# Performance work log

Measured on AMD Instinct MI355X. Metric: run time of the kernel, lower is better.

## Reference

```python
import jax, jax.numpy as jnp
import numpy as np

B = 32768
IN_DIM = 768
HIDDENS = [2048, 1024, 512]
EMBED_DIM = 128
NUM_EMB = 1024
DEPTH = 3


def setup_inputs() -> dict:
    key = jax.random.key(0)
    ks = jax.random.split(key, 20)
    d = {"x": jax.random.normal(ks[0], (B, IN_DIM), dtype=jnp.float32)}
    # Encoder: in -> h0 -> h1 -> h2 -> embed  (weights stored as [in, out])
    enc_dims = [IN_DIM] + HIDDENS + [EMBED_DIM]
    for i in range(4):
        fan_in = enc_dims[i]
        d[f"enc_W{i+1}"] = jax.random.normal(ks[1 + i], (enc_dims[i], enc_dims[i + 1]), dtype=jnp.float32) / np.sqrt(fan_in)
        d[f"enc_b{i+1}"] = jnp.zeros((enc_dims[i + 1],), dtype=jnp.float32)
    # Decoder: embed -> h0 -> h1 -> h2 -> in
    dec_dims = [EMBED_DIM] + HIDDENS + [IN_DIM]
    for i in range(4):
        fan_in = dec_dims[i]
        d[f"dec_W{i+1}"] = jax.random.normal(ks[5 + i], (dec_dims[i], dec_dims[i + 1]), dtype=jnp.float32) / np.sqrt(fan_in)
        d[f"dec_b{i+1}"] = jnp.zeros((dec_dims[i + 1],), dtype=jnp.float32)
    # Codebook (nn.Embedding weight, initialized ~ N(0,1) as in the module)
    d["codebook"] = jax.random.normal(ks[9], (NUM_EMB, EMBED_DIM), dtype=jnp.float32)
    return d


def _encoder(x, W1, b1, W2, b2, W3, b3, W4, b4):
    x = jax.nn.relu(x @ W1 + b1)
    x = jax.nn.relu(x @ W2 + b2)
    x = jax.nn.relu(x @ W3 + b3)
    return x @ W4 + b4


def _decoder(x, W1, b1, W2, b2, W3, b3, W4, b4):
    x = jax.nn.relu(x @ W1 + b1)
    x = jax.nn.relu(x @ W2 + b2)
    x = jax.nn.relu(x @ W3 + b3)
    return x @ W4 + b4


def reference(x,
              enc_W1, enc_b1, enc_W2, enc_b2, enc_W3, enc_b3, enc_W4, enc_b4,
              dec_W1, dec_b1, dec_W2, dec_b2, dec_W3, dec_b3, dec_W4, dec_b4,
              codebook):
    z = _encoder(x, enc_W1, enc_b1, enc_W2, enc_b2, enc_W3, enc_b3, enc_W4, enc_b4)
    z_det = jax.lax.stop_gradient(z)

    cb_sq = jnp.sum(codebook * codebook, axis=1)  # [K]
    residue = z_det
    z_hat = jnp.zeros_like(z_det)
    codes = []
    for _ in range(DEPTH):  # residual quantization loop
        # squared L2 distances [B, K]
        dist = (jnp.sum(residue * residue, axis=1, keepdims=True)
                + cb_sq
                - 2.0 * residue @ codebook.T)
        idx = jnp.argmin(dist, axis=1)          # [B]
        codes.append(idx)
        z_hat = z_hat + codebook[idx]           # gather codebook vectors
        residue = z_det - z_hat
    all_codes = jnp.stack(codes, axis=1)        # [B, DEPTH] int

    # straight-through estimator: forward uses z_hat, grad flows through z
    z_flow = z + jax.lax.stop_gradient(z_hat - z)
    x_recon = _decoder(z_flow, dec_W1, dec_b1, dec_W2, dec_b2, dec_W3, dec_b3, dec_W4, dec_b4)
    return (x_recon, all_codes)
```

## Files before the change

kernel.cpp:

```cpp
#include <hip/hip_runtime.h>

#define FLT_MAX_C 3.402823466e+38f

typedef __attribute__((ext_vector_type(8))) __bf16 bf16x8;
typedef __attribute__((ext_vector_type(4))) float f32x4;

static __device__ __forceinline__ ushort f2bf(float x) {
    union { float f; unsigned u; } v; v.f = x;
    unsigned r = (v.u + 0x7FFFu + ((v.u >> 16) & 1u)) >> 16;
    return (ushort)r;
}

static __device__ __forceinline__ void xcd_swz(int& bx, int& by) {
    const int gx = gridDim.x;
    const int nwg = gx * gridDim.y;
    const int bid = blockIdx.y * gx + blockIdx.x;
    const int q = nwg >> 3, r = nwg & 7;
    const int xcd = bid & 7, lid = bid >> 3;
    const int swz = (xcd < r ? xcd * (q + 1) : r * (q + 1) + (xcd - r) * q) + lid;
    bx = swz % gx;
    by = swz / gx;
}

template<bool RELU>
__device__ __forceinline__ void gemm_f32_dev(
    const float* __restrict__ A, const float* __restrict__ W,
    const float* __restrict__ bias, float* __restrict__ C, int K, int N,
    int bxi, int byi)
{
    __shared__ float As[8][128];
    __shared__ float Bs[8][132];
    const int tid = threadIdx.x;
    const int bm = byi << 7;
    const int bn = bxi << 7;

    const int la_row = tid >> 1;
    const int la_k   = (tid & 1) << 2;
    const int lb_row = tid >> 5;
    const int lb_col = (tid & 31) << 2;
    const int tm4 = (tid >> 4) << 2;
    const int tn4 = (tid & 15) << 2;

    float acc[8][8];
    #pragma unroll
    for (int i = 0; i < 8; ++i)
        #pragma unroll
        for (int j = 0; j < 8; ++j) acc[i][j] = 0.f;

    const float* aptr = A + (size_t)(bm + la_row) * K + la_k;
    const float* bptr = W + (size_t)lb_row * N + bn + lb_col;

    float4 av = *(const float4*)(aptr);
    float4 bv = *(const float4*)(bptr);

    for (int k0 = 0; k0 < K; k0 += 8) {
        __syncthreads();
        As[la_k + 0][la_row] = av.x;
        As[la_k + 1][la_row] = av.y;
        As[la_k + 2][la_row] = av.z;
        As[la_k + 3][la_row] = av.w;
        *(float4*)(&Bs[lb_row][lb_col]) = bv;
        __syncthreads();
        if (k0 + 8 < K) {
            av = *(const float4*)(aptr + k0 + 8);
            bv = *(const float4*)(bptr + (size_t)(k0 + 8) * N);
        }
        #pragma unroll
        for (int kk = 0; kk < 8; ++kk) {
            float a[8], b[8];
            *(float4*)(a)     = *(const float4*)(&As[kk][tm4]);
            *(float4*)(a + 4) = *(const float4*)(&As[kk][tm4 + 64]);
            *(float4*)(b)     = *(const float4*)(&Bs[kk][tn4]);
            *(float4*)(b + 4) = *(const float4*)(&Bs[kk][tn4 + 64]);
            #pragma unroll
            for (int i = 0; i < 8; ++i)
                #pragma unroll
                for (int j = 0; j < 8; ++j)
                    acc[i][j] = fmaf(a[i], b[j], acc[i][j]);
        }
    }

    float bv0[8];
    #pragma unroll
    for (int j = 0; j < 8; ++j)
        bv0[j] = bias[bn + tn4 + (j < 4 ? j : 60 + j)];

    #pragma unroll
    for (int i = 0; i < 8; ++i) {
        int row = bm + tm4 + (i < 4 ? i : 60 + i);
        float* cp = C + (size_t)row * N + bn + tn4;
        float4 v0, v1;
        v0.x = acc[i][0] + bv0[0]; v0.y = acc[i][1] + bv0[1];
        v0.z = acc[i][2] + bv0[2]; v0.w = acc[i][3] + bv0[3];
        v1.x = acc[i][4] + bv0[4]; v1.y = acc[i][5] + bv0[5];
        v1.z = acc[i][6] + bv0[6]; v1.w = acc[i][7] + bv0[7];
        if (RELU) {
            v0.x = fmaxf(v0.x, 0.f); v0.y = fmaxf(v0.y, 0.f);
            v0.z = fmaxf(v0.z, 0.f); v0.w = fmaxf(v0.w, 0.f);
            v1.x = fmaxf(v1.x, 0.f); v1.y = fmaxf(v1.y, 0.f);
            v1.z = fmaxf(v1.z, 0.f); v1.w = fmaxf(v1.w, 0.f);
        }
        *(float4*)(cp) = v0;
        *(float4*)(cp + 64) = v1;
    }
}

template<bool RELU>
__device__ __forceinline__ void gemm_f32_wide_dev(
    const float* __restrict__ A, const float* __restrict__ W,
    const float* __restrict__ bias, float* __restrict__ C, int K, int N,
    int bxi, int byi, void* smem)
{
    float (*As)[128] = (float(*)[128])smem;
    float (*Bs)[260] = (float(*)[260])((char*)smem + 4096);
    const int tid = threadIdx.x;
    const int bm = byi << 7;
    const int bn = bxi << 8;

    const int la_row = tid >> 1;
    const int la_k   = (tid & 1) << 2;
    const int tm4 = (tid >> 4) << 2;
    const int tn4 = (tid & 15) << 2;
    const int bf_row  = tid >> 6;
    const int bf_col4 = (tid & 63) << 2;

    float acc[8][16];
    #pragma unroll
    for (int i = 0; i < 8; ++i)
        #pragma unroll
        for (int j = 0; j < 16; ++j) acc[i][j] = 0.f;

    const float* aptr = A + (size_t)(bm + la_row) * K + la_k;
    const float* bptr = W + (size_t)bf_row * N + bn + bf_col4;

    float4 av = *(const float4*)(aptr);
    float4 bv0 = *(const float4*)(bptr);
    float4 bv1 = *(const float4*)(bptr + (size_t)4 * N);

    for (int k0 = 0; k0 < K; k0 += 8) {
        __syncthreads();
        As[la_k + 0][la_row] = av.x;
        As[la_k + 1][la_row] = av.y;
        As[la_k + 2][la_row] = av.z;
        As[la_k + 3][la_row] = av.w;
        *(float4*)(&Bs[bf_row][bf_col4])     = bv0;
        *(float4*)(&Bs[bf_row + 4][bf_col4]) = bv1;
        __syncthreads();
        if (k0 + 8 < K) {
            av  = *(const float4*)(aptr + k0 + 8);
            bv0 = *(const float4*)(bptr + (size_t)(k0 + 8) * N);
            bv1 = *(const float4*)(bptr + (size_t)(k0 + 12) * N);
        }
        #pragma unroll
        for (int kk = 0; kk < 8; ++kk) {
            float a[8], b[16];
            *(float4*)(a)      = *(const float4*)(&As[kk][tm4]);
            *(float4*)(a + 4)  = *(const float4*)(&As[kk][tm4 + 64]);
            #pragma unroll
            for (int q = 0; q < 4; ++q)
                *(float4*)(b + q * 4) = *(const float4*)(&Bs[kk][tn4 + 64 * q]);
            #pragma unroll
            for (int i = 0; i < 8; ++i)
                #pragma unroll
                for (int j = 0; j < 16; ++j)
                    acc[i][j] = fmaf(a[i], b[j], acc[i][j]);
        }
    }

    float bb[16];
    #pragma unroll
    for (int q = 0; q < 4; ++q)
        #pragma unroll
        for (int jj = 0; jj < 4; ++jj)
            bb[q * 4 + jj] = bias[bn + tn4 + 64 * q + jj];

    #pragma unroll
    for (int i = 0; i < 8; ++i) {
        int row = bm + tm4 + (i < 4 ? i : 60 + i);
        float* cp = C + (size_t)row * N + bn + tn4;
        #pragma unroll
        for (int q = 0; q < 4; ++q) {
            float4 v;
            v.x = acc[i][q * 4 + 0] + bb[q * 4 + 0];
            v.y = acc[i][q * 4 + 1] + bb[q * 4 + 1];
            v.z = acc[i][q * 4 + 2] + bb[q * 4 + 2];
            v.w = acc[i][q * 4 + 3] + bb[q * 4 + 3];
            if (RELU) {
                v.x = fmaxf(v.x, 0.f); v.y = fmaxf(v.y, 0.f);
                v.z = fmaxf(v.z, 0.f); v.w = fmaxf(v.w, 0.f);
            }
            *(float4*)(cp + 64 * q) = v;
        }
    }
}

template<bool RELU>
__device__ __forceinline__ void gemm_f32_64_dev(
    const float* __restrict__ A, const float* __restrict__ W,
    const float* __restrict__ bias, float* __restrict__ C, int K, int N,
    int bxi, int byi)
{
    __shared__ float As[16][64];
    __shared__ float Bs[16][132];
    const int tid = threadIdx.x;
    const int bm = byi << 6;
    const int bn = bxi << 7;

    const int la_row = tid & 63;
    const int la_k   = (tid >> 6) << 2;
    const int lb_row = tid >> 5;
    const int lb_col = (tid & 31) << 2;
    const int tr = tid >> 4;
    const int tc = tid & 15;

    float acc[4][8];
    #pragma unroll
    for (int i = 0; i < 4; ++i)
        #pragma unroll
        for (int j = 0; j < 8; ++j) acc[i][j] = 0.f;

    const float* aptr = A + (size_t)(bm + la_row) * K + la_k;
    const float* bptr = W + (size_t)lb_row * N + bn + lb_col;

    float4 av = *(const float4*)(aptr);
    float4 bv0 = *(const float4*)(bptr);
    float4 bv1 = *(const float4*)(bptr + (size_t)8 * N);

    for (int k0 = 0; k0 < K; k0 += 16) {
        __syncthreads();
        As[la_k + 0][la_row] = av.x;
        As[la_k + 1][la_row] = av.y;
        As[la_k + 2][la_row] = av.z;
        As[la_k + 3][la_row] = av.w;
        *(float4*)(&Bs[lb_row][lb_col]) = bv0;
        *(float4*)(&Bs[lb_row + 8][lb_col]) = bv1;
        __syncthreads();
        if (k0 + 16 < K) {
            av  = *(const float4*)(aptr + k0 + 16);
            bv0 = *(const float4*)(bptr + (size_t)(k0 + 16) * N);
            bv1 = *(const float4*)(bptr + (size_t)(k0 + 24) * N);
        }
        #pragma unroll
        for (int kk = 0; kk < 16; ++kk) {
            float a[4], b[8];
            *(float4*)(a) = *(const float4*)(&As[kk][tr << 2]);
            *(float4*)(b)     = *(const float4*)(&Bs[kk][tc << 2]);
            *(float4*)(b + 4) = *(const float4*)(&Bs[kk][(tc << 2) + 64]);
            #pragma unroll
            for (int i = 0; i < 4; ++i)
                #pragma unroll
                for (int j = 0; j < 8; ++j)
                    acc[i][j] = fmaf(a[i], b[j], acc[i][j]);
        }
    }

    float bb[8];
    #pragma unroll
    for (int j = 0; j < 8; ++j)
        bb[j] = bias[bn + (tc << 2) + (j < 4 ? j : 60 + j)];

    #pragma unroll
    for (int i = 0; i < 4; ++i) {
        float* cp = C + (size_t)(bm + (tr << 2) + i) * N + bn + (tc << 2);
        float4 v0, v1;
        v0.x = acc[i][0] + bb[0]; v0.y = acc[i][1] + bb[1];
        v0.z = acc[i][2] + bb[2]; v0.w = acc[i][3] + bb[3];
        v1.x = acc[i][4] + bb[4]; v1.y = acc[i][5] + bb[5];
        v1.z = acc[i][6] + bb[6]; v1.w = acc[i][7] + bb[7];
        if (RELU) {
            v0.x = fmaxf(v0.x, 0.f); v0.y = fmaxf(v0.y, 0.f);
            v0.z = fmaxf(v0.z, 0.f); v0.w = fmaxf(v0.w, 0.f);
            v1.x = fmaxf(v1.x, 0.f); v1.y = fmaxf(v1.y, 0.f);
            v1.z = fmaxf(v1.z, 0.f); v1.w = fmaxf(v1.w, 0.f);
        }
        *(float4*)(cp) = v0;
        *(float4*)(cp + 64) = v1;
    }
}

template<bool RELU, bool OUTF32>
__device__ __forceinline__ void gemm_bf16_dev(
    const ushort* __restrict__ A, const ushort* __restrict__ Wt,
    const float* __restrict__ bias, void* __restrict__ C, int K, int N,
    int bxi, int byi)
{
    __shared__ __align__(16) ushort As[2][128][32];
    __shared__ __align__(16) ushort Bs[2][128][32];
    const int tid  = threadIdx.x;
    const int lane = tid & 63;
    const int wv   = tid >> 6;
    const int wm   = (wv >> 1) << 6;
    const int wn   = (wv & 1) << 6;
    const int bm   = byi << 7;
    const int bn   = bxi << 7;
    const int lr   = lane & 15;
    const int lh   = lane >> 4;

    f32x4 acc[4][4];
    #pragma unroll
    for (int m = 0; m < 4; ++m)
        #pragma unroll
        for (int n = 0; n < 4; ++n) acc[m][n] = (f32x4){0.f, 0.f, 0.f, 0.f};

    auto stage = [&](int t, int bsel) {
        const int k0 = t << 5;
        #pragma unroll
        for (int i = 0; i < 2; ++i) {
            const int blk = i * 4 + wv;
            const int f   = blk * 64 + lane;
            const int r   = f >> 2;
            const int cbyte = (f & 3) << 4;
            const char* sa = (const char*)A  + (((size_t)(bm + r) * K + k0) << 1) + cbyte;
            const char* sb = (const char*)Wt + (((size_t)(bn + r) * K + k0) << 1) + cbyte;
            __builtin_amdgcn_global_load_lds((const void*)sa,
                (void*)((char*)(&As[bsel][0][0]) + blk * 1024), 16, 0, 0);
            __builtin_amdgcn_global_load_lds((const void*)sb,
                (void*)((char*)(&Bs[bsel][0][0]) + blk * 1024), 16, 0, 0);
        }
    };

    const int nt = K >> 5;
    stage(0, 0);
    __syncthreads();

    for (int t = 0; t < nt; ++t) {
        const int b = t & 1;
        if (t + 1 < nt) stage(t + 1, b ^ 1);
        bf16x8 af[4], bfr[4];
        #pragma unroll
        for (int m = 0; m < 4; ++m)
            af[m] = *(const bf16x8*)&As[b][wm + m * 16 + lr][lh * 8];
        #pragma unroll
        for (int n = 0; n < 4; ++n)
            bfr[n] = *(const bf16x8*)&Bs[b][wn + n * 16 + lr][lh * 8];
        #pragma unroll
        for (int m = 0; m < 4; ++m)
            #pragma unroll
            for (int n = 0; n < 4; ++n)
                acc[m][n] = __builtin_amdgcn_mfma_f32_16x16x32_bf16(
                    af[m], bfr[n], acc[m][n], 0, 0, 0);
        __syncthreads();
    }

    #pragma unroll
    for (int n = 0; n < 4; ++n) {
        const int col = bn + wn + n * 16 + lr;
        const float bcol = bias[col];
        #pragma unroll
        for (int m = 0; m < 4; ++m) {
            #pragma unroll
            for (int i = 0; i < 4; ++i) {
                const int row = bm + wm + m * 16 + lh * 4 + i;
                float v = acc[m][n][i] + bcol;
                if (RELU) v = fmaxf(v, 0.f);
                if (OUTF32) ((float*)C)[(size_t)row * N + col] = v;
                else        ((ushort*)C)[(size_t)row * N + col] = f2bf(v);
            }
        }
    }
}

__device__ __forceinline__ void wt_convert_dev(
    const float* __restrict__ W, ushort* __restrict__ Wt, int K, int N,
    int bx, int by, void* smem)
{
    ushort (*t)[65] = (ushort(*)[65])smem;
    const int kb = by << 6, nb = bx << 6;
    const int c  = threadIdx.x & 63;
    const int r0 = (threadIdx.x >> 6) << 4;
    #pragma unroll
    for (int i = 0; i < 16; ++i)
        t[r0 + i][c] = f2bf(W[(size_t)(kb + r0 + i) * N + nb + c]);
    __syncthreads();
    #pragma unroll
    for (int i = 0; i < 16; ++i)
        Wt[(size_t)(nb + r0 + i) * K + kb + c] = t[c][r0 + i];
}

__device__ __forceinline__ void prep_dispatch(
    int b,
    const float* dW1, const float* dW2, const float* dW3, const float* dW4,
    ushort* Wt1, ushort* Wt2, ushort* Wt3, ushort* Wt4,
    const float* cb, float* sq, float* cbt, void* smem)
{
    if (b < 64)  { wt_convert_dev(dW1, Wt1, 128,  2048, b % 32, b / 32, smem); return; }
    b -= 64;
    if (b < 512) { wt_convert_dev(dW2, Wt2, 2048, 1024, b % 16, b / 16, smem); return; }
    b -= 512;
    if (b < 128) { wt_convert_dev(dW3, Wt3, 1024, 512,  b % 8,  b / 8,  smem); return; }
    b -= 128;
    if (b < 96)  { wt_convert_dev(dW4, Wt4, 512,  768,  b % 12, b / 12, smem); return; }
    b -= 96;
    if (b < 4) {
        int k = b * 256 + threadIdx.x;
        const float* r = cb + ((size_t)k << 7);
        float s = 0.f;
        #pragma unroll 8
        for (int d = 0; d < 128; ++d) s = fmaf(r[d], r[d], s);
        sq[k] = s;
        return;
    }
    b -= 4;
    {
        float (*t)[65] = (float(*)[65])smem;
        const int kb = (b % 16) << 6;
        const int db = (b / 16) << 6;
        const int c  = threadIdx.x & 63;
        const int r0 = (threadIdx.x >> 6) << 4;
        #pragma unroll
        for (int i = 0; i < 16; ++i)
            t[r0 + i][c] = cb[(size_t)(kb + r0 + i) * 128 + db + c];
        __syncthreads();
        #pragma unroll
        for (int i = 0; i < 16; ++i)
            cbt[(size_t)(db + r0 + i) * 1024 + kb + c] = t[c][r0 + i];
    }
}

__global__ __launch_bounds__(256) void enc1_prep(
    const float* A, const float* W, const float* b, float* C, int encb,
    const float* dW1, const float* dW2, const float* dW3, const float* dW4,
    ushort* Wt1, ushort* Wt2, ushort* Wt3, ushort* Wt4,
    const float* cb, float* sq, float* cbt)
{
    __shared__ __align__(16) char pool[16640];
    const int bid = blockIdx.x;
    if (bid < encb) {
        gemm_f32_wide_dev<true>(A, W, b, C, 768, 2048, bid & 7, bid >> 3, pool);
    } else {
        prep_dispatch(bid - encb, dW1, dW2, dW3, dW4, Wt1, Wt2, Wt3, Wt4,
                      cb, sq, cbt, pool);
    }
}

__global__ __launch_bounds__(256) void enc2_gemm(const float* A, const float* W, const float* b, float* C)
{ __shared__ __align__(16) char pool[12416];
  int bx, by; xcd_swz(bx, by);
  gemm_f32_wide_dev<true>(A, W, b, C, 2048, 1024, bx, by, pool); }
__global__ __launch_bounds__(256) void enc3_gemm(const float* A, const float* W, const float* b, float* C)
{ int bx, by; xcd_swz(bx, by); gemm_f32_dev<true>(A, W, b, C, 1024, 512, bx, by); }
__global__ __launch_bounds__(256) void enc4_gemm(const float* A, const float* W, const float* b, float* C)
{ int bx, by; xcd_swz(bx, by); gemm_f32_64_dev<false>(A, W, b, C, 512, 128, bx, by); }
__global__ __launch_bounds__(256) void dec1_gemm(const ushort* A, const ushort* Wt, const float* b, void* C)
{ int bx, by; xcd_swz(bx, by); gemm_bf16_dev<true, false>(A, Wt, b, C, 128, 2048, bx, by); }
__global__ __launch_bounds__(256) void dec2_gemm(const ushort* A, const ushort* Wt, const float* b, void* C)
{ int bx, by; xcd_swz(bx, by); gemm_bf16_dev<true, false>(A, Wt, b, C, 2048, 1024, bx, by); }
__global__ __launch_bounds__(256) void dec3_gemm(const ushort* A, const ushort* Wt, const float* b, void* C)
{ int bx, by; xcd_swz(bx, by); gemm_bf16_dev<true, false>(A, Wt, b, C, 1024, 512, bx, by); }
__global__ __launch_bounds__(256) void dec4_gemm(const ushort* A, const ushort* Wt, const float* b, void* C)
{ int bx, by; xcd_swz(bx, by); gemm_bf16_dev<false, true>(A, Wt, b, C, 512, 768, bx, by); }

__global__ __launch_bounds__(256) void rq_all(
    const float* __restrict__ z, const float* __restrict__ cbt,
    const float* __restrict__ sq, const float* __restrict__ cb,
    ushort* __restrict__ ZHb, float* __restrict__ codes)
{
    __shared__ float As[128][68];
    __shared__ float Bs[32][132];
    __shared__ float sqs[1024];
    __shared__ float rrs[64];

    const int tid = threadIdx.x;
    const int bm  = blockIdx.x << 6;
    const int tr  = tid >> 4;
    const int c   = tid & 15;
    const int tn4 = c << 2;
    const int lb_row = tid >> 5;
    const int lb_col = (tid & 31) << 2;

    #pragma unroll
    for (int i = 0; i < 4; ++i) sqs[tid + (i << 8)] = sq[tid + (i << 8)];

    float zh[4][8];
    #pragma unroll
    for (int i = 0; i < 4; ++i) {
        const int r_  = (tr << 2) + i;
        const float* zp = z + (size_t)(bm + r_) * 128 + (c << 3);
        float4 z0 = *(const float4*)(zp);
        float4 z1 = *(const float4*)(zp + 4);
        #pragma unroll
        for (int j = 0; j < 8; ++j) zh[i][j] = 0.f;
        As[(c << 3) + 0][r_] = z0.x; As[(c << 3) + 1][r_] = z0.y;
        As[(c << 3) + 2][r_] = z0.z; As[(c << 3) + 3][r_] = z0.w;
        As[(c << 3) + 4][r_] = z1.x; As[(c << 3) + 5][r_] = z1.y;
        As[(c << 3) + 6][r_] = z1.z; As[(c << 3) + 7][r_] = z1.w;
        float p = z0.x * z0.x;
        p = fmaf(z0.y, z0.y, p); p = fmaf(z0.z, z0.z, p);
        p = fmaf(z0.w, z0.w, p); p = fmaf(z1.x, z1.x, p);
        p = fmaf(z1.y, z1.y, p); p = fmaf(z1.z, z1.z, p);
        p = fmaf(z1.w, z1.w, p);
        #pragma unroll
        for (int o = 8; o >= 1; o >>= 1) p += __shfl_xor(p, o);
        if (c == 0) rrs[r_] = p;
    }
    __syncthreads();

    for (int t = 0; t < 3; ++t) {
        float rr_[4];
        #pragma unroll
        for (int i = 0; i < 4; ++i) rr_[i] = rrs[(tr << 2) + i];

        float best_d[4] = {FLT_MAX_C, FLT_MAX_C, FLT_MAX_C, FLT_MAX_C};
        int   best_i[4] = {0, 0, 0, 0};

        for (int bx = 0; bx < 8; ++bx) {
            const int bn = bx << 7;
            const float* bptr = cbt + (size_t)lb_row * 1024 + bn + lb_col;
            float4 bv0 = *(const float4*)(bptr);
            float4 bv1 = *(const float4*)(bptr + (size_t)8  * 1024);
            float4 bv2 = *(const float4*)(bptr + (size_t)16 * 1024);
            float4 bv3 = *(const float4*)(bptr + (size_t)24 * 1024);

            float acc[4][8];
            #pragma unroll
            for (int i = 0; i < 4; ++i)
                #pragma unroll
                for (int j = 0; j < 8; ++j) acc[i][j] = 0.f;

            for (int k0 = 0; k0 < 128; k0 += 32) {
                __syncthreads();
                *(float4*)(&Bs[lb_row +  0][lb_col]) = bv0;
                *(float4*)(&Bs[lb_row +  8][lb_col]) = bv1;
                *(float4*)(&Bs[lb_row + 16][lb_col]) = bv2;
                *(float4*)(&Bs[lb_row + 24][lb_col]) = bv3;
                __syncthreads();
                if (k0 + 32 < 128) {
                    bv0 = *(const float4*)(bptr + (size_t)(k0 + 32) * 1024);
                    bv1 = *(const float4*)(bptr + (size_t)(k0 + 40) * 1024);
                    bv2 = *(const float4*)(bptr + (size_t)(k0 + 48) * 1024);
                    bv3 = *(const float4*)(bptr + (size_t)(k0 + 56) * 1024);
                }
                #pragma unroll
                for (int kk = 0; kk < 32; ++kk) {
                    float a[4], b[8];
                    *(float4*)(a)     = *(const float4*)(&As[k0 + kk][tr << 2]);
                    *(float4*)(b)     = *(const float4*)(&Bs[kk][tn4]);
                    *(float4*)(b + 4) = *(const float4*)(&Bs[kk][tn4 + 64]);
                    #pragma unroll
                    for (int i = 0; i < 4; ++i)
                        #pragma unroll
                        for (int j = 0; j < 8; ++j)
                            acc[i][j] = fmaf(a[i], b[j], acc[i][j]);
                }
            }
            #pragma unroll
            for (int i = 0; i < 4; ++i) {
                #pragma unroll
                for (int j = 0; j < 8; ++j) {
                    const int col = bn + tn4 + (j < 4 ? j : 60 + j);
                    float d = (rr_[i] + sqs[col]) - 2.f * acc[i][j];
                    if (d < best_d[i]) { best_d[i] = d; best_i[i] = col; }
                }
            }
        }

        #pragma unroll
        for (int i = 0; i < 4; ++i) {
            float bd = best_d[i]; int bi = best_i[i];
            #pragma unroll
            for (int o = 8; o >= 1; o >>= 1) {
                float od = __shfl_xor(bd, o);
                int   oi = __shfl_xor(bi, o);
                if (od < bd || (od == bd && oi < bi)) { bd = od; bi = oi; }
            }
            best_i[i] = bi;
        }

        __syncthreads();

        #pragma unroll
        for (int i = 0; i < 4; ++i) {
            const int r_  = (tr << 2) + i;
            const int row = bm + r_;
            if (c == 0) codes[(size_t)row * 3 + t] = (float)best_i[i];

            const float* cbp = cb + ((size_t)best_i[i] << 7) + (c << 3);
            float4 c0 = *(const float4*)(cbp);
            float4 c1 = *(const float4*)(cbp + 4);
            zh[i][0] += c0.x; zh[i][1] += c0.y;
            zh[i][2] += c0.z; zh[i][3] += c0.w;
            zh[i][4] += c1.x; zh[i][5] += c1.y;
            zh[i][6] += c1.z; zh[i][7] += c1.w;

            if (t < 2) {
                const float* zp = z + (size_t)row * 128 + (c << 3);
                float4 z0 = *(const float4*)(zp);
                float4 z1 = *(const float4*)(zp + 4);
                float r0 = z0.x - zh[i][0], r1 = z0.y - zh[i][1];
                float r2 = z0.z - zh[i][2], r3 = z0.w - zh[i][3];
                float r4 = z1.x - zh[i][4], r5 = z1.y - zh[i][5];
                float r6 = z1.z - zh[i][6], r7 = z1.w - zh[i][7];
                As[(c << 3) + 0][r_] = r0; As[(c << 3) + 1][r_] = r1;
                As[(c << 3) + 2][r_] = r2; As[(c << 3) + 3][r_] = r3;
                As[(c << 3) + 4][r_] = r4; As[(c << 3) + 5][r_] = r5;
                As[(c << 3) + 6][r_] = r6; As[(c << 3) + 7][r_] = r7;
                float p = r0 * r0;
                p = fmaf(r1, r1, p); p = fmaf(r2, r2, p);
                p = fmaf(r3, r3, p); p = fmaf(r4, r4, p);
                p = fmaf(r5, r5, p); p = fmaf(r6, r6, p);
                p = fmaf(r7, r7, p);
                #pragma unroll
                for (int o = 8; o >= 1; o >>= 1) p += __shfl_xor(p, o);
                if (c == 0) rrs[r_] = p;
            } else {
                ushort4 o0, o1;
                o0.x = f2bf(zh[i][0]); o0.y = f2bf(zh[i][1]);
                o0.z = f2bf(zh[i][2]); o0.w = f2bf(zh[i][3]);
                o1.x = f2bf(zh[i][4]); o1.y = f2bf(zh[i][5]);
                o1.z = f2bf(zh[i][6]); o1.w = f2bf(zh[i][7]);
                ushort* zbp = ZHb + (size_t)row * 128 + (c << 3);
                *(ushort4*)(zbp)     = o0;
                *(ushort4*)(zbp + 4) = o1;
            }
        }
        if (t < 2) __syncthreads();
    }
}

extern "C" void kernel_launch(void* const* d_in, const int* in_sizes, int n_in,
                              void* d_out, int out_size, void* d_ws, size_t ws_size,
                              hipStream_t stream)
{
    const float* x   = (const float*)d_in[0];
    const float* eW1 = (const float*)d_in[1];
    const float* eb1 = (const float*)d_in[2];
    const float* eW2 = (const float*)d_in[3];
    const float* eb2 = (const float*)d_in[4];
    const float* eW3 = (const float*)d_in[5];
    const float* eb3 = (const float*)d_in[6];
    const float* eW4 = (const float*)d_in[7];
    const float* eb4 = (const float*)d_in[8];
    const float* dW1 = (const float*)d_in[9];
    const float* db1 = (const float*)d_in[10];
    const float* dW2 = (const float*)d_in[11];
    const float* db2 = (const float*)d_in[12];
    const float* dW3 = (const float*)d_in[13];
    const float* db3 = (const float*)d_in[14];
    const float* dW4 = (const float*)d_in[15];
    const float* db4 = (const float*)d_in[16];
    const float* cb  = (const float*)d_in[17];

    float* out   = (float*)d_out;
    float* codes = out + (size_t)32768 * 768;

    ushort* Wt1 = (ushort*)d_ws;
    ushort* Wt2 = Wt1 + (size_t)2048 * 128;
    ushort* Wt3 = Wt2 + (size_t)1024 * 2048;
    ushort* Wt4 = Wt3 + (size_t)512 * 1024;
    float*  sq  = (float*)(Wt4 + (size_t)768 * 512);
    float*  cbt = sq + 1024;
    float*  act = cbt + (size_t)128 * 1024;
    const size_t fixed_b = (char*)act - (char*)d_ws;

    int mc = 32768;
    while (mc > 1024) {
        if (fixed_b + (size_t)mc * 15104 <= ws_size) break;
        mc >>= 1;
    }

    float*  R1  = act;
    float*  R2  = R1 + (size_t)mc * 2048;
    float*  R3  = R2 + (size_t)mc * 1024;
    float*  RZ  = R3 + (size_t)mc * 512;
    ushort* ZHb = (ushort*)(RZ + (size_t)mc * 128);
    ushort* D1  = (ushort*)R1;
    ushort* D2  = (ushort*)R2;
    ushort* D3  = (ushort*)R3;

    const int mg = mc >> 7;
    bool first = true;
    for (int r0 = 0; r0 < 32768; r0 += mc) {
        const float* xi     = x     + (size_t)r0 * 768;
        float*       outi   = out   + (size_t)r0 * 768;
        float*       codesi = codes + (size_t)r0 * 3;
        const int encb = 8 * mg;
        const int prepb = first ? 836 : 0;
        enc1_prep<<<encb + prepb, 256, 0, stream>>>(
            xi, eW1, eb1, R1, encb,
            dW1, dW2, dW3, dW4, Wt1, Wt2, Wt3, Wt4, cb, sq, cbt);
        first = false;
        enc2_gemm<<<dim3( 4, mg), 256, 0, stream>>>(R1, eW2, eb2, R2);
        enc3_gemm<<<dim3( 4, mg), 256, 0, stream>>>(R2, eW3, eb3, R3);
        enc4_gemm<<<dim3( 1, mc >> 6), 256, 0, stream>>>(R3, eW4, eb4, RZ);
        rq_all<<<mc >> 6, 256, 0, stream>>>(RZ, cbt, sq, cb, ZHb, codesi);
        dec1_gemm<<<dim3(16, mg), 256, 0, stream>>>(ZHb, Wt1, db1, D1);
        dec2_gemm<<<dim3( 8, mg), 256, 0, stream>>>(D1,  Wt2, db2, D2);
        dec3_gemm<<<dim3( 4, mg), 256, 0, stream>>>(D2,  Wt3, db3, D3);
        dec4_gemm<<<dim3( 6, mg), 256, 0, stream>>>(D3,  Wt4, db4, outi);
    }
}
```

Baseline: 3.763 ms.

## Double-buffer LDS in wide fp32 GEMM and use it for enc3

The wide fp32 GEMM tile now keeps two LDS buffers. The next K-slice is written into the alternate buffer after compute, so each iteration needs one barrier instead of two. The enc3 layer switches from the 128x128 tile kernel to the 128x256 wide kernel with half as many column blocks, and the old narrow GEMM is deleted. LDS per block grows, which may lower occupancy, and enc3 now launches fewer workgroups.

```diff
diff --git a/kernel.cpp b/kernel.cpp
--- a/kernel.cpp
+++ b/kernel.cpp
@@ -23,96 +23,13 @@
 }
 
 template<bool RELU>
-__device__ __forceinline__ void gemm_f32_dev(
-    const float* __restrict__ A, const float* __restrict__ W,
-    const float* __restrict__ bias, float* __restrict__ C, int K, int N,
-    int bxi, int byi)
-{
-    __shared__ float As[8][128];
-    __shared__ float Bs[8][132];
-    const int tid = threadIdx.x;
-    const int bm = byi << 7;
-    const int bn = bxi << 7;
-
-    const int la_row = tid >> 1;
-    const int la_k   = (tid & 1) << 2;
-    const int lb_row = tid >> 5;
-    const int lb_col = (tid & 31) << 2;
-    const int tm4 = (tid >> 4) << 2;
-    const int tn4 = (tid & 15) << 2;
-
-    float acc[8][8];
-    #pragma unroll
-    for (int i = 0; i < 8; ++i)
-        #pragma unroll
-        for (int j = 0; j < 8; ++j) acc[i][j] = 0.f;
-
-    const float* aptr = A + (size_t)(bm + la_row) * K + la_k;
-    const float* bptr = W + (size_t)lb_row * N + bn + lb_col;
-
-    float4 av = *(const float4*)(aptr);
-    float4 bv = *(const float4*)(bptr);
-
-    for (int k0 = 0; k0 < K; k0 += 8) {
-        __syncthreads();
-        As[la_k + 0][la_row] = av.x;
-        As[la_k + 1][la_row] = av.y;
-        As[la_k + 2][la_row] = av.z;
-        As[la_k + 3][la_row] = av.w;
-        *(float4*)(&Bs[lb_row][lb_col]) = bv;
-        __syncthreads();
-        if (k0 + 8 < K) {
-            av = *(const float4*)(aptr + k0 + 8);
-            bv = *(const float4*)(bptr + (size_t)(k0 + 8) * N);
-        }
-        #pragma unroll
-        for (int kk = 0; kk < 8; ++kk) {
-            float a[8], b[8];
-            *(float4*)(a)     = *(const float4*)(&As[kk][tm4]);
-            *(float4*)(a + 4) = *(const float4*)(&As[kk][tm4 + 64]);
-            *(float4*)(b)     = *(const float4*)(&Bs[kk][tn4]);
-            *(float4*)(b + 4) = *(const float4*)(&Bs[kk][tn4 + 64]);
-            #pragma unroll
-            for (int i = 0; i < 8; ++i)
-                #pragma unroll
-                for (int j = 0; j < 8; ++j)
-                    acc[i][j] = fmaf(a[i], b[j], acc[i][j]);
-        }
-    }
-
-    float bv0[8];
-    #pragma unroll
-    for (int j = 0; j < 8; ++j)
-        bv0[j] = bias[bn + tn4 + (j < 4 ? j : 60 + j)];
-
-    #pragma unroll
-    for (int i = 0; i < 8; ++i) {
-        int row = bm + tm4 + (i < 4 ? i : 60 + i);
-        float* cp = C + (size_t)row * N + bn + tn4;
-        float4 v0, v1;
-        v0.x = acc[i][0] + bv0[0]; v0.y = acc[i][1] + bv0[1];
-        v0.z = acc[i][2] + bv0[2]; v0.w = acc[i][3] + bv0[3];
-        v1.x = acc[i][4] + bv0[4]; v1.y = acc[i][5] + bv0[5];
-        v1.z = acc[i][6] + bv0[6]; v1.w = acc[i][7] + bv0[7];
-        if (RELU) {
-            v0.x = fmaxf(v0.x, 0.f); v0.y = fmaxf(v0.y, 0.f);
-            v0.z = fmaxf(v0.z, 0.f); v0.w = fmaxf(v0.w, 0.f);
-            v1.x = fmaxf(v1.x, 0.f); v1.y = fmaxf(v1.y, 0.f);
-            v1.z = fmaxf(v1.z, 0.f); v1.w = fmaxf(v1.w, 0.f);
-        }
-        *(float4*)(cp) = v0;
-        *(float4*)(cp + 64) = v1;
-    }
-}
-
-template<bool RELU>
 __device__ __forceinline__ void gemm_f32_wide_dev(
     const float* __restrict__ A, const float* __restrict__ W,
     const float* __restrict__ bias, float* __restrict__ C, int K, int N,
     int bxi, int byi, void* smem)
 {
-    float (*As)[128] = (float(*)[128])smem;
-    float (*Bs)[260] = (float(*)[260])((char*)smem + 4096);
+    float (*As)[8][128] = (float(*)[8][128])smem;
+    float (*Bs)[8][260] = (float(*)[8][260])((char*)smem + 8192);
     const int tid = threadIdx.x;
     const int bm = byi << 7;
     const int bn = bxi << 8;
@@ -136,35 +53,46 @@
     float4 av = *(const float4*)(aptr);
     float4 bv0 = *(const float4*)(bptr);
     float4 bv1 = *(const float4*)(bptr + (size_t)4 * N);
-
-    for (int k0 = 0; k0 < K; k0 += 8) {
-        __syncthreads();
-        As[la_k + 0][la_row] = av.x;
-        As[la_k + 1][la_row] = av.y;
-        As[la_k + 2][la_row] = av.z;
-        As[la_k + 3][la_row] = av.w;
-        *(float4*)(&Bs[bf_row][bf_col4])     = bv0;
-        *(float4*)(&Bs[bf_row + 4][bf_col4]) = bv1;
-        __syncthreads();
-        if (k0 + 8 < K) {
-            av  = *(const float4*)(aptr + k0 + 8);
-            bv0 = *(const float4*)(bptr + (size_t)(k0 + 8) * N);
-            bv1 = *(const float4*)(bptr + (size_t)(k0 + 12) * N);
+    As[0][la_k + 0][la_row] = av.x;
+    As[0][la_k + 1][la_row] = av.y;
+    As[0][la_k + 2][la_row] = av.z;
+    As[0][la_k + 3][la_row] = av.w;
+    *(float4*)(&Bs[0][bf_row][bf_col4])     = bv0;
+    *(float4*)(&Bs[0][bf_row + 4][bf_col4]) = bv1;
+    __syncthreads();
+
+    const int nt = K >> 3;
+    for (int t = 0; t < nt; ++t) {
+        const int b = t & 1;
+        if (t + 1 < nt) {
+            const int k0n = (t + 1) << 3;
+            av  = *(const float4*)(aptr + k0n);
+            bv0 = *(const float4*)(bptr + (size_t)k0n * N);
+            bv1 = *(const float4*)(bptr + (size_t)(k0n + 4) * N);
         }
         #pragma unroll
         for (int kk = 0; kk < 8; ++kk) {
-            float a[8], b[16];
-            *(float4*)(a)      = *(const float4*)(&As[kk][tm4]);
-            *(float4*)(a + 4)  = *(const float4*)(&As[kk][tm4 + 64]);
+            float a[8], bfr[16];
+            *(float4*)(a)      = *(const float4*)(&As[b][kk][tm4]);
+            *(float4*)(a + 4)  = *(const float4*)(&As[b][kk][tm4 + 64]);
             #pragma unroll
             for (int q = 0; q < 4; ++q)
-                *(float4*)(b + q * 4) = *(const float4*)(&Bs[kk][tn4 + 64 * q]);
+                *(float4*)(bfr + q * 4) = *(const float4*)(&Bs[b][kk][tn4 + 64 * q]);
             #pragma unroll
             for (int i = 0; i < 8; ++i)
                 #pragma unroll
                 for (int j = 0; j < 16; ++j)
-                    acc[i][j] = fmaf(a[i], b[j], acc[i][j]);
-        }
+                    acc[i][j] = fmaf(a[i], bfr[j], acc[i][j]);
+        }
+        if (t + 1 < nt) {
+            As[b ^ 1][la_k + 0][la_row] = av.x;
+            As[b ^ 1][la_k + 1][la_row] = av.y;
+            As[b ^ 1][la_k + 2][la_row] = av.z;
+            As[b ^ 1][la_k + 3][la_row] = av.w;
+            *(float4*)(&Bs[b ^ 1][bf_row][bf_col4])     = bv0;
+            *(float4*)(&Bs[b ^ 1][bf_row + 4][bf_col4]) = bv1;
+        }
+        __syncthreads();
     }
 
     float bb[16];
@@ -271,7 +199,7 @@
             v0.x = fmaxf(v0.x, 0.f); v0.y = fmaxf(v0.y, 0.f);
             v0.z = fmaxf(v0.z, 0.f); v0.w = fmaxf(v0.w, 0.f);
             v1.x = fmaxf(v1.x, 0.f); v1.y = fmaxf(v1.y, 0.f);
-            v1.z = fmaxf(v1.z, 0.f); v1.w = fmaxf(v1.w, 0.f);
+            v1.w = fmaxf(v1.w, 0.f); v1.z = fmaxf(v1.z, 0.f);
         }
         *(float4*)(cp) = v0;
         *(float4*)(cp + 64) = v1;
@@ -423,7 +351,7 @@
     ushort* Wt1, ushort* Wt2, ushort* Wt3, ushort* Wt4,
     const float* cb, float* sq, float* cbt)
 {
-    __shared__ __align__(16) char pool[16640];
+    __shared__ __align__(16) char pool[24832];
     const int bid = blockIdx.x;
     if (bid < encb) {
         gemm_f32_wide_dev<true>(A, W, b, C, 768, 2048, bid & 7, bid >> 3, pool);
@@ -434,11 +362,13 @@
 }
 
 __global__ __launch_bounds__(256) void enc2_gemm(const float* A, const float* W, const float* b, float* C)
-{ __shared__ __align__(16) char pool[12416];
+{ __shared__ __align__(16) char pool[24832];
   int bx, by; xcd_swz(bx, by);
   gemm_f32_wide_dev<true>(A, W, b, C, 2048, 1024, bx, by, pool); }
 __global__ __launch_bounds__(256) void enc3_gemm(const float* A, const float* W, const float* b, float* C)
-{ int bx, by; xcd_swz(bx, by); gemm_f32_dev<true>(A, W, b, C, 1024, 512, bx, by); }
+{ __shared__ __align__(16) char pool[24832];
+  int bx, by; xcd_swz(bx, by);
+  gemm_f32_wide_dev<true>(A, W, b, C, 1024, 512, bx, by, pool); }
 __global__ __launch_bounds__(256) void enc4_gemm(const float* A, const float* W, const float* b, float* C)
 { int bx, by; xcd_swz(bx, by); gemm_f32_64_dev<false>(A, W, b, C, 512, 128, bx, by); }
 __global__ __launch_bounds__(256) void dec1_gemm(const ushort* A, const ushort* Wt, const float* b, void* C)
@@ -680,7 +610,7 @@
             dW1, dW2, dW3, dW4, Wt1, Wt2, Wt3, Wt4, cb, sq, cbt);
         first = false;
         enc2_gemm<<<dim3( 4, mg), 256, 0, stream>>>(R1, eW2, eb2, R2);
-        enc3_gemm<<<dim3( 4, mg), 256, 0, stream>>>(R2, eW3, eb3, R3);
+        enc3_gemm<<<dim3( 2, mg), 256, 0, stream>>>(R2, eW3, eb3, R3);
         enc4_gemm<<<dim3( 1, mc >> 6), 256, 0, stream>>>(R3, eW4, eb4, RZ);
         rq_all<<<mc >> 6, 256, 0, stream>>>(RZ, cbt, sq, cb, ZHb, codesi);
         dec1_gemm<<<dim3(16, mg), 256, 0, stream>>>(ZHb, Wt1, db1, D1);
```

Result: slower. 5.086 ms (+35.1%).
